# Optimization experiments

Measured on AMD Instinct MI355X. Metric: run time of the kernel, lower is better.

Reference implementation:

```python
import jax, jax.numpy as jnp
import numpy as np

HEADS = 2

def gat_layer(x, edge_index, W, att, bias):
    # x: [N, Fin], W: [H*C, Fin], att: [1, H, 2C], bias: [C]
    N = x.shape[0]
    C = bias.shape[0]
    # add self loops (source_to_target: x_j from row 0, aggregate onto row 1)
    loop = jnp.arange(N, dtype=edge_index.dtype)
    src = jnp.concatenate([edge_index[0], loop])
    dst = jnp.concatenate([edge_index[1], loop])
    h = (x @ W.T).reshape(N, HEADS, C)          # [N, H, C]
    x_j = h[src]                                 # [E, H, C]
    x_i = h[dst]                                 # [E, H, C]
    x_cat = jnp.concatenate([x_i, x_j], axis=-1) # [E, H, 2C]
    alpha = (x_cat * att).sum(-1)                # [E, H]
    alpha = jnp.where(alpha >= 0, alpha, 0.2 * alpha)  # leaky_relu(0.2)
    # NOTE: module uses a global (not per-destination) normalization
    alpha = jnp.exp(alpha - alpha.max())
    alpha = alpha / (alpha.sum(axis=0, keepdims=True) + 1e-10)
    msg = x_j * alpha[..., None]                 # [E, H, C]
    aggr = jax.ops.segment_sum(msg, dst, num_segments=N)  # [N, H, C]
    return aggr.mean(axis=1) + bias              # [N, C]

def setup_inputs() -> dict:
    key = jax.random.key(0)
    ks = jax.random.split(key, 7)
    N, Fin, C = 50000, 128, 64
    E = 800000
    x = jax.random.normal(ks[0], (N, Fin), dtype=jnp.float32)
    edge_index = jax.random.randint(ks[1], (2, E), 0, N, dtype=jnp.int64)
    W1 = jax.random.normal(ks[2], (HEADS * C, Fin), dtype=jnp.float32) * 0.05
    att1 = jax.random.normal(ks[3], (1, HEADS, 2 * C), dtype=jnp.float32) * 0.05
    b1 = jnp.zeros((C,), dtype=jnp.float32)
    W2 = jax.random.normal(ks[4], (HEADS * C, C), dtype=jnp.float32) * 0.05
    att2 = jax.random.normal(ks[5], (1, HEADS, 2 * C), dtype=jnp.float32) * 0.05
    b2 = jnp.zeros((C,), dtype=jnp.float32)
    return {"x": x, "edge_index": edge_index, "W1": W1, "att1": att1,
            "b1": b1, "W2": W2, "att2": att2, "b2": b2}

def reference(x, edge_index, W1, att1, b1, W2, att2, b2):
    h = gat_layer(x, edge_index, W1, att1, b1)
    h = jax.nn.relu(h)
    # F.dropout with training flag: treated as eval (identity) for determinism
    out = gat_layer(h, edge_index, W2, att2, b2)
    return out
```

## Files before the change

### kernel.cpp

```cpp
#include <hip/hip_runtime.h>
#include <hip/hip_bf16.h>
#include <math.h>


#define NHIST 1264
#define NZ    256
#define NSCAT 1792

using short8 = __attribute__((ext_vector_type(8))) short;
using f32x4  = __attribute__((ext_vector_type(4))) float;

__device__ __forceinline__ unsigned f2bf(float x) {
  unsigned u = __float_as_uint(x);
  return (u + 0x7fffu + ((u >> 16) & 1u)) >> 16;
}
__device__ __forceinline__ float bflo(unsigned p) { return __uint_as_float(p << 16); }
__device__ __forceinline__ float bfhi(unsigned p) { return __uint_as_float(p & 0xffff0000u); }

__global__ __launch_bounds__(256) void init_ws(
    int* __restrict__ cursor, float* __restrict__ Z, int N) {
  int tid = blockIdx.x * 256 + threadIdx.x;
  int stride = gridDim.x * 256;
  for (int i = tid; i < N; i += stride) cursor[i] = 0;
  if (tid < 4) Z[tid] = 0.f;
}

template <int FIN>
__global__ __launch_bounds__(256) void gemm_mfma(
    const float* __restrict__ x, const float* __restrict__ W,
    const float* __restrict__ att, unsigned* __restrict__ hq,
    float* __restrict__ si, float* __restrict__ sj,
    int N,
    const int* __restrict__ dstE, int* __restrict__ deg,
    int E, int ntiles, int step) {
  const int tid = threadIdx.x;

  if ((int)blockIdx.x >= ntiles) {
    int bid = blockIdx.x - ntiles;
    int p = bid & 7, sub = bid >> 3;
    int nsub = NHIST >> 3;
    int lo = p * step, hi = lo + step;
    int stride = nsub * 256;
    for (int e = sub * 256 + tid; e < E; e += stride) {
      int d = dstE[e];
      if (d >= lo && d < hi) atomicAdd(&deg[d], 1);
    }
    return;
  }

  constexpr int KS = FIN / 32;
  constexpr int CPR = FIN / 8;
  constexpr int NCHUNK = 128 * CPR;

  __shared__ unsigned short wlds[128 * FIN];

  const int w    = tid >> 6;
  const int lane = tid & 63;
  const int cl   = lane & 15;
  const int grp  = lane >> 4;
  const int n0   = blockIdx.x * 64;

  const int arow = n0 + w * 16 + cl;
  const bool avalid = arow < N;
  float4 av0[KS], av1[KS];
#pragma unroll
  for (int ks = 0; ks < KS; ++ks) {
    av0[ks] = make_float4(0.f, 0.f, 0.f, 0.f);
    av1[ks] = av0[ks];
    if (avalid) {
      const float4* xp =
          (const float4*)(x + (size_t)arow * FIN + ks * 32 + grp * 8);
      av0[ks] = xp[0];
      av1[ks] = xp[1];
    }
  }

  const float4* W4 = (const float4*)W;
  for (int c = tid; c < NCHUNK; c += 256) {
    int row = c / CPR;
    int cc  = c & (CPR - 1);
    float4 lo = W4[c * 2];
    float4 hi = W4[c * 2 + 1];
    unsigned short* dst = &wlds[row * FIN + ((cc ^ (row & (CPR - 1))) * 8)];
    *(uint4*)dst = make_uint4(
        f2bf(lo.x) | (f2bf(lo.y) << 16), f2bf(lo.z) | (f2bf(lo.w) << 16),
        f2bf(hi.x) | (f2bf(hi.y) << 16), f2bf(hi.z) | (f2bf(hi.w) << 16));
  }
  __syncthreads();

  short8 afrag[KS];
#pragma unroll
  for (int ks = 0; ks < KS; ++ks) {
    union { short8 s8; unsigned u[4]; } af;
    af.u[0] = f2bf(av0[ks].x) | (f2bf(av0[ks].y) << 16);
    af.u[1] = f2bf(av0[ks].z) | (f2bf(av0[ks].w) << 16);
    af.u[2] = f2bf(av1[ks].x) | (f2bf(av1[ks].y) << 16);
    af.u[3] = f2bf(av1[ks].z) | (f2bf(av1[ks].w) << 16);
    afrag[ks] = af.s8;
  }

  f32x4 acc[8];
#pragma unroll
  for (int ct = 0; ct < 8; ++ct) acc[ct] = (f32x4){0.f, 0.f, 0.f, 0.f};

  const int swz = cl & (CPR - 1);
#pragma unroll
  for (int ks = 0; ks < KS; ++ks) {
#pragma unroll
    for (int ct = 0; ct < 8; ++ct) {
      const unsigned short* bp =
          &wlds[(ct * 16 + cl) * FIN + (((ks * 4 + grp) ^ swz) * 8)];
      short8 bfrag = *(const short8*)bp;
      acc[ct] = __builtin_amdgcn_mfma_f32_16x16x32_bf16(afrag[ks], bfrag,
                                                        acc[ct], 0, 0, 0);
    }
  }

  float ai[8], aj[8];
#pragma unroll
  for (int ct = 0; ct < 8; ++ct) {
    int hd = ct >> 2;
    int cw = (ct & 3) * 16 + cl;
    ai[ct] = att[hd * 128 + cw];
    aj[ct] = att[hd * 128 + 64 + cw];
  }

#pragma unroll
  for (int r = 0; r < 4; ++r) {
    int node = n0 + w * 16 + grp * 4 + r;
    float s0i = 0.f, s0j = 0.f, s1i = 0.f, s1j = 0.f;
    unsigned wpk[4];
#pragma unroll
    for (int ct = 0; ct < 4; ++ct) {
      float v0 = acc[ct][r];
      float v1 = acc[ct + 4][r];
      s0i += v0 * ai[ct];
      s0j += v0 * aj[ct];
      s1i += v1 * ai[ct + 4];
      s1j += v1 * aj[ct + 4];
      wpk[ct] = f2bf(v0) | (f2bf(v1) << 16);
    }
#pragma unroll
    for (int off = 8; off; off >>= 1) {
      s0i += __shfl_xor(s0i, off, 64);
      s0j += __shfl_xor(s0j, off, 64);
      s1i += __shfl_xor(s1i, off, 64);
      s1j += __shfl_xor(s1j, off, 64);
    }
    if (node < N) {
#pragma unroll
      for (int ct = 0; ct < 4; ++ct)
        hq[(size_t)node * 64 + ct * 16 + cl] = wpk[ct];
      if (cl == 0) {
        si[node * 2 + 0] = s0i;
        si[node * 2 + 1] = s1i;
        sj[node * 2 + 0] = s0j;
        sj[node * 2 + 1] = s1j;
      }
    }
  }
}

__device__ __forceinline__ void z_edge_body(
    const int* __restrict__ srcE, const int* __restrict__ dstE,
    const float2* __restrict__ si2, const float2* __restrict__ sj2,
    float* __restrict__ Zp, int E, int Etot, int tid0, int stride) {
  float z0 = 0.f, z1 = 0.f;
  for (int e = tid0; e < Etot; e += stride) {
    int s, d;
    if (e < E) { s = srcE[e]; d = dstE[e]; } else { s = d = e - E; }
    float2 siv = si2[d];
    float2 sjv = sj2[s];
    float a0 = siv.x + sjv.x;
    float a1 = siv.y + sjv.y;
    a0 = a0 >= 0.f ? a0 : 0.2f * a0;
    a1 = a1 >= 0.f ? a1 : 0.2f * a1;
    z0 += __expf(a0); z1 += __expf(a1);
  }
  __shared__ float r0[4], r1[4];
  int lane = threadIdx.x & 63, w = threadIdx.x >> 6;
#pragma unroll
  for (int off = 32; off; off >>= 1) {
    z0 += __shfl_down(z0, off, 64);
    z1 += __shfl_down(z1, off, 64);
  }
  if (lane == 0) { r0[w] = z0; r1[w] = z1; }
  __syncthreads();
  if (threadIdx.x == 0) {
    atomicAdd(&Zp[0], r0[0] + r0[1] + r0[2] + r0[3]);
    atomicAdd(&Zp[1], r1[0] + r1[1] + r1[2] + r1[3]);
  }
}

__global__ __launch_bounds__(256) void z_edge(
    const int* __restrict__ srcE, const int* __restrict__ dstE,
    const float2* __restrict__ si2, const float2* __restrict__ sj2,
    float* __restrict__ Zp, int E, int Etot) {
  z_edge_body(srcE, dstE, si2, sj2, Zp, E, Etot,
              blockIdx.x * 256 + threadIdx.x, gridDim.x * 256);
}

__global__ __launch_bounds__(256) void scan_blocks(
    const int* __restrict__ deg, int* __restrict__ rowptr,
    int* __restrict__ bsum, int N) {
  __shared__ int ts[256];
  int b = blockIdx.x, t = threadIdx.x;
  int base = b * 1024 + t * 4;
  int v[4];
#pragma unroll
  for (int j = 0; j < 4; ++j) v[j] = (base + j < N) ? deg[base + j] : 0;
  int tot = v[0] + v[1] + v[2] + v[3];
  ts[t] = tot;
  __syncthreads();
#pragma unroll
  for (int off = 1; off < 256; off <<= 1) {
    int x = (t >= off) ? ts[t - off] : 0;
    __syncthreads();
    ts[t] += x;
    __syncthreads();
  }
  int run = ts[t] - tot;
#pragma unroll
  for (int j = 0; j < 4; ++j) {
    if (base + j < N) rowptr[base + j] = run;
    run += v[j];
  }
  if (t == 255) bsum[b] = ts[255];
}

__global__ __launch_bounds__(256) void scan_finish(
    int* __restrict__ rowptr, const int* __restrict__ bsum,
    int* __restrict__ cursor, int N, int Eall, int nb) {
  __shared__ int pre[256];
  if (threadIdx.x == 0) {
    int run = 0;
    for (int i = 0; i < nb; ++i) { pre[i] = run; run += bsum[i]; }
  }
  __syncthreads();
  int tid = blockIdx.x * blockDim.x + threadIdx.x;
  int stride = gridDim.x * blockDim.x;
  for (int i = tid; i < N; i += stride) {
    int v = rowptr[i] + pre[i >> 10];
    rowptr[i] = v;
    cursor[i] = v;
  }
  if (tid == 0) rowptr[N] = Eall;
}

__global__ __launch_bounds__(256) void scatter_z(
    const int* __restrict__ srcE, const int* __restrict__ dstE,
    int* __restrict__ cursor, int* __restrict__ esrc,
    const float2* __restrict__ si2, const float2* __restrict__ sj2,
    float* __restrict__ Zp, int E, int Etot, int step) {
  if ((int)blockIdx.x < NZ) {
    z_edge_body(srcE, dstE, si2, sj2, Zp, E, Etot,
                blockIdx.x * 256 + threadIdx.x, NZ * 256);
    return;
  }
  const int bid = blockIdx.x - NZ;
  const int p = bid & 7;
  const int sub = bid >> 3;
  const int nsub = NSCAT >> 3;
  const int lo = p * step;
  const int hi = lo + step;
  int stride = nsub * 256;
  for (int e = sub * 256 + threadIdx.x; e < E; e += stride) {
    int d = dstE[e];
    if (d >= lo && d < hi) {
      int s = srcE[e];
      int pos = atomicAdd(&cursor[d], 1);
      esrc[pos] = s;
    }
  }
}

__global__ __launch_bounds__(256) void csr_aggregate(
    const int* __restrict__ rowptr, const int* __restrict__ esrc,
    const unsigned* __restrict__ hq, const float2* __restrict__ si2,
    const float2* __restrict__ sj2, const float* __restrict__ Zp,
    const float* __restrict__ bias, float* __restrict__ out,
    int N, int do_relu) {
  int lane = threadIdx.x & 63;
  int wid = (blockIdx.x * blockDim.x + threadIdx.x) >> 6;
  int nw = (gridDim.x * blockDim.x) >> 6;
  float z0 = 1.f / (Zp[0] + 1e-10f);
  float z1 = 1.f / (Zp[1] + 1e-10f);
  float bv = bias[lane];
  for (int n0 = wid; n0 < N; n0 += nw) {
    int n = __builtin_amdgcn_readfirstlane(n0);
    int beg = rowptr[n], end = rowptr[n + 1];
    float2 siv = si2[n];
    float acc0, acc1;
    {
      float2 jv = sj2[n];
      unsigned p = hq[(size_t)n * 64 + lane];
      float a0 = siv.x + jv.x, a1 = siv.y + jv.y;
      a0 = a0 >= 0.f ? a0 : 0.2f * a0;
      a1 = a1 >= 0.f ? a1 : 0.2f * a1;
      acc0 = bflo(p) * __expf(a0);
      acc1 = bfhi(p) * __expf(a1);
    }
    int k = beg;
    for (; k + 4 <= end; k += 4) {
      int s0 = esrc[k], s1 = esrc[k + 1], s2 = esrc[k + 2], s3 = esrc[k + 3];
      float2 j0 = sj2[s0], j1 = sj2[s1], j2 = sj2[s2], j3 = sj2[s3];
      unsigned p0 = hq[(size_t)s0 * 64 + lane];
      unsigned p1 = hq[(size_t)s1 * 64 + lane];
      unsigned p2 = hq[(size_t)s2 * 64 + lane];
      unsigned p3 = hq[(size_t)s3 * 64 + lane];
      float a00 = siv.x + j0.x, a01 = siv.y + j0.y;
      float a10 = siv.x + j1.x, a11 = siv.y + j1.y;
      float a20 = siv.x + j2.x, a21 = siv.y + j2.y;
      float a30 = siv.x + j3.x, a31 = siv.y + j3.y;
      a00 = a00 >= 0.f ? a00 : 0.2f * a00;  a01 = a01 >= 0.f ? a01 : 0.2f * a01;
      a10 = a10 >= 0.f ? a10 : 0.2f * a10;  a11 = a11 >= 0.f ? a11 : 0.2f * a11;
      a20 = a20 >= 0.f ? a20 : 0.2f * a20;  a21 = a21 >= 0.f ? a21 : 0.2f * a21;
      a30 = a30 >= 0.f ? a30 : 0.2f * a30;  a31 = a31 >= 0.f ? a31 : 0.2f * a31;
      float w00 = __expf(a00), w01 = __expf(a01);
      float w10 = __expf(a10), w11 = __expf(a11);
      float w20 = __expf(a20), w21 = __expf(a21);
      float w30 = __expf(a30), w31 = __expf(a31);
      acc0 += bflo(p0) * w00 + bflo(p1) * w10 + bflo(p2) * w20 + bflo(p3) * w30;
      acc1 += bfhi(p0) * w01 + bfhi(p1) * w11 + bfhi(p2) * w21 + bfhi(p3) * w31;
    }
    for (; k < end; ++k) {
      int s = esrc[k];
      float2 jv = sj2[s];
      unsigned p = hq[(size_t)s * 64 + lane];
      float a0 = siv.x + jv.x, a1 = siv.y + jv.y;
      a0 = a0 >= 0.f ? a0 : 0.2f * a0;
      a1 = a1 >= 0.f ? a1 : 0.2f * a1;
      acc0 += bflo(p) * __expf(a0);
      acc1 += bfhi(p) * __expf(a1);
    }
    float r = 0.5f * (acc0 * z0 + acc1 * z1) + bv;
    if (do_relu) r = fmaxf(r, 0.f);
    out[(size_t)n * 64 + lane] = r;
  }
}

extern "C" void kernel_launch(void* const* d_in, const int* in_sizes, int n_in,
                              void* d_out, int out_size, void* d_ws, size_t ws_size,
                              hipStream_t stream) {
  const float* x    = (const float*)d_in[0];
  const int*   ei   = (const int*)d_in[1];
  const float* W1   = (const float*)d_in[2];
  const float* att1 = (const float*)d_in[3];
  const float* b1   = (const float*)d_in[4];
  const float* W2   = (const float*)d_in[5];
  const float* att2 = (const float*)d_in[6];
  const float* b2   = (const float*)d_in[7];
  float* out = (float*)d_out;

  const int N = in_sizes[0] / 128;
  const int E = in_sizes[1] / 2;
  const int Etot = E + N;
  const int* srcE = ei;
  const int* dstE = ei + E;

  unsigned* hq = (unsigned*)d_ws;
  float* si    = (float*)(hq + (size_t)N * 64);
  float* sj    = si + (size_t)N * 2;
  float* Z     = sj + (size_t)N * 2;
  float* x2    = Z + 4;
  int* rowptr  = (int*)(x2 + (size_t)N * 64);
  int* cursor  = rowptr + (N + 1);
  int* esrc    = cursor + N;
  int* bsum    = esrc + E;

  dim3 blk(256);
  int nb = (N + 1023) / 1024;
  int ntiles = (N + 63) / 64;
  int step = (N + 7) / 8;

  init_ws<<<128, blk, 0, stream>>>(cursor, Z, N);
  gemm_mfma<128><<<ntiles + NHIST, blk, 0, stream>>>(
      x, W1, att1, hq, si, sj, N, dstE, cursor, E, ntiles, step);
  scan_blocks<<<nb, blk, 0, stream>>>(cursor, rowptr, bsum, N);
  scan_finish<<<256, blk, 0, stream>>>(rowptr, bsum, cursor, N, E, nb);
  scatter_z<<<NZ + NSCAT, blk, 0, stream>>>(
      srcE, dstE, cursor, esrc, (const float2*)si, (const float2*)sj,
      Z, E, Etot, step);
  csr_aggregate<<<4096, blk, 0, stream>>>(rowptr, esrc, hq, (const float2*)si,
                                          (const float2*)sj, Z, b1, x2, N, 1);
  gemm_mfma<64><<<ntiles, blk, 0, stream>>>(
      x2, W2, att2, hq, si, sj, N, dstE, cursor, E, ntiles, step);
  z_edge<<<NZ, blk, 0, stream>>>(srcE, dstE, (const float2*)si,
                                 (const float2*)sj, Z + 2, E, Etot);
  csr_aggregate<<<4096, blk, 0, stream>>>(rowptr, esrc, hq, (const float2*)si,
                                          (const float2*)sj, Z + 2, b2, out, N, 0);
}
```

Measured before the change: 283.1 us.

## Build degree histogram in LDS partials and pre-convert weights to bf16 once

The degree count moves from global atomics by 1264 blocks to 64 blocks that each keep a range histogram in shared memory and write per-group partial counts, which scan_blocks then sums across 8 groups. Zeroing the cursor is no longer needed, and init_ws now converts W1 and W2 to bf16 once, so every GEMM block copies pre-packed weights into LDS without converting them. This cuts global atomic contention and repeated conversion work. In exchange it adds an 8xN partial buffer, extra reads in the scan, and only 64 histogram blocks each scanning E/8 edges, which could lengthen the first GEMM launch.

```diff
diff --git a/kernel.cpp b/kernel.cpp
--- a/kernel.cpp
+++ b/kernel.cpp
@@ -3,7 +3,9 @@
 #include <math.h>
 
 
-#define NHIST 1264
+#define NHISTB 64
+#define HP 8
+#define HRANGE_MAX 6272
 #define NZ    256
 #define NSCAT 1792
 
@@ -18,32 +20,47 @@
 __device__ __forceinline__ float bfhi(unsigned p) { return __uint_as_float(p & 0xffff0000u); }
 
 __global__ __launch_bounds__(256) void init_ws(
-    int* __restrict__ cursor, float* __restrict__ Z, int N) {
+    const float* __restrict__ W1, const float* __restrict__ W2,
+    unsigned short* __restrict__ wbf1, unsigned short* __restrict__ wbf2,
+    float* __restrict__ Z) {
   int tid = blockIdx.x * 256 + threadIdx.x;
   int stride = gridDim.x * 256;
-  for (int i = tid; i < N; i += stride) cursor[i] = 0;
+  for (int i = tid; i < 128 * 128; i += stride)
+    wbf1[i] = (unsigned short)f2bf(W1[i]);
+  for (int i = tid; i < 128 * 64; i += stride)
+    wbf2[i] = (unsigned short)f2bf(W2[i]);
   if (tid < 4) Z[tid] = 0.f;
 }
 
 template <int FIN>
 __global__ __launch_bounds__(256) void gemm_mfma(
-    const float* __restrict__ x, const float* __restrict__ W,
+    const float* __restrict__ x, const unsigned short* __restrict__ Wb,
     const float* __restrict__ att, unsigned* __restrict__ hq,
     float* __restrict__ si, float* __restrict__ sj,
     int N,
-    const int* __restrict__ dstE, int* __restrict__ deg,
-    int E, int ntiles, int step) {
+    const int* __restrict__ dstE, int* __restrict__ partial,
+    int E, int nhistb, int hstep) {
   const int tid = threadIdx.x;
 
-  if ((int)blockIdx.x >= ntiles) {
-    int bid = blockIdx.x - ntiles;
-    int p = bid & 7, sub = bid >> 3;
-    int nsub = NHIST >> 3;
-    int lo = p * step, hi = lo + step;
-    int stride = nsub * 256;
-    for (int e = sub * 256 + tid; e < E; e += stride) {
-      int d = dstE[e];
-      if (d >= lo && d < hi) atomicAdd(&deg[d], 1);
+  constexpr int WB = 128 * FIN * 2;
+  constexpr int SMEM = (WB > HRANGE_MAX * 4) ? WB : HRANGE_MAX * 4;
+  __shared__ __align__(16) unsigned char smem[SMEM];
+
+  if ((int)blockIdx.x < nhistb) {
+    int* lhist = (int*)smem;
+    const int p = blockIdx.x & (HP - 1);
+    const int g = blockIdx.x >> 3;
+    const int lo = p * hstep;
+    for (int i = tid; i < hstep; i += 256) lhist[i] = 0;
+    __syncthreads();
+    for (int e = g * 256 + tid; e < E; e += 8 * 256) {
+      int d = dstE[e] - lo;
+      if ((unsigned)d < (unsigned)hstep) atomicAdd(&lhist[d], 1);
+    }
+    __syncthreads();
+    for (int i = tid; i < hstep; i += 256) {
+      int node = lo + i;
+      if (node < N) partial[(size_t)g * N + node] = lhist[i];
     }
     return;
   }
@@ -52,13 +69,13 @@
   constexpr int CPR = FIN / 8;
   constexpr int NCHUNK = 128 * CPR;
 
-  __shared__ unsigned short wlds[128 * FIN];
+  unsigned short* wlds = (unsigned short*)smem;
 
   const int w    = tid >> 6;
   const int lane = tid & 63;
   const int cl   = lane & 15;
   const int grp  = lane >> 4;
-  const int n0   = blockIdx.x * 64;
+  const int n0   = (blockIdx.x - nhistb) * 64;
 
   const int arow = n0 + w * 16 + cl;
   const bool avalid = arow < N;
@@ -75,16 +92,11 @@
     }
   }
 
-  const float4* W4 = (const float4*)W;
+  const uint4* Wb4 = (const uint4*)Wb;
   for (int c = tid; c < NCHUNK; c += 256) {
     int row = c / CPR;
     int cc  = c & (CPR - 1);
-    float4 lo = W4[c * 2];
-    float4 hi = W4[c * 2 + 1];
-    unsigned short* dst = &wlds[row * FIN + ((cc ^ (row & (CPR - 1))) * 8)];
-    *(uint4*)dst = make_uint4(
-        f2bf(lo.x) | (f2bf(lo.y) << 16), f2bf(lo.z) | (f2bf(lo.w) << 16),
-        f2bf(hi.x) | (f2bf(hi.y) << 16), f2bf(hi.z) | (f2bf(hi.w) << 16));
+    *(uint4*)&wlds[row * FIN + ((cc ^ (row & (CPR - 1))) * 8)] = Wb4[c];
   }
   __syncthreads();
 
@@ -201,14 +213,20 @@
 }
 
 __global__ __launch_bounds__(256) void scan_blocks(
-    const int* __restrict__ deg, int* __restrict__ rowptr,
+    const int* __restrict__ partial, int* __restrict__ rowptr,
     int* __restrict__ bsum, int N) {
   __shared__ int ts[256];
   int b = blockIdx.x, t = threadIdx.x;
   int base = b * 1024 + t * 4;
   int v[4];
 #pragma unroll
-  for (int j = 0; j < 4; ++j) v[j] = (base + j < N) ? deg[base + j] : 0;
+  for (int j = 0; j < 4; ++j) {
+    v[j] = 0;
+    if (base + j < N) {
+#pragma unroll
+      for (int g = 0; g < 8; ++g) v[j] += partial[(size_t)g * N + base + j];
+    }
+  }
   int tot = v[0] + v[1] + v[2] + v[3];
   ts[t] = tot;
   __syncthreads();
@@ -367,16 +385,21 @@
   int* cursor  = rowptr + (N + 1);
   int* esrc    = cursor + N;
   int* bsum    = esrc + E;
+  uintptr_t wp = ((uintptr_t)(bsum + 256) + 15) & ~(uintptr_t)15;
+  unsigned short* wbf1 = (unsigned short*)wp;
+  unsigned short* wbf2 = wbf1 + 128 * 128;
+  int* partial = (int*)(wbf2 + 128 * 64);
 
   dim3 blk(256);
   int nb = (N + 1023) / 1024;
   int ntiles = (N + 63) / 64;
   int step = (N + 7) / 8;
-
-  init_ws<<<128, blk, 0, stream>>>(cursor, Z, N);
-  gemm_mfma<128><<<ntiles + NHIST, blk, 0, stream>>>(
-      x, W1, att1, hq, si, sj, N, dstE, cursor, E, ntiles, step);
-  scan_blocks<<<nb, blk, 0, stream>>>(cursor, rowptr, bsum, N);
+  int hstep = (N + HP - 1) / HP;
+
+  init_ws<<<64, blk, 0, stream>>>(W1, W2, wbf1, wbf2, Z);
+  gemm_mfma<128><<<NHISTB + ntiles, blk, 0, stream>>>(
+      x, wbf1, att1, hq, si, sj, N, dstE, partial, E, NHISTB, hstep);
+  scan_blocks<<<nb, blk, 0, stream>>>(partial, rowptr, bsum, N);
   scan_finish<<<256, blk, 0, stream>>>(rowptr, bsum, cursor, N, E, nb);
   scatter_z<<<NZ + NSCAT, blk, 0, stream>>>(
       srcE, dstE, cursor, esrc, (const float2*)si, (const float2*)sj,
@@ -384,7 +407,7 @@
   csr_aggregate<<<4096, blk, 0, stream>>>(rowptr, esrc, hq, (const float2*)si,
                                           (const float2*)sj, Z, b1, x2, N, 1);
   gemm_mfma<64><<<ntiles, blk, 0, stream>>>(
-      x2, W2, att2, hq, si, sj, N, dstE, cursor, E, ntiles, step);
+      x2, wbf2, att2, hq, si, sj, N, dstE, partial, E, 0, hstep);
   z_edge<<<NZ, blk, 0, stream>>>(srcE, dstE, (const float2*)si,
                                  (const float2*)sj, Z + 2, E, Etot);
   csr_aggregate<<<4096, blk, 0, stream>>>(rowptr, esrc, hq, (const float2*)si,
```

Result: slower. 363.9 us (+28.5%).
